# Optimization experiments

Hardware: AMD Instinct MI355X
Metric: run time of the kernel (lower is better)

The kernel has to match this reference:

```python
import jax, jax.numpy as jnp
import numpy as np

N = 100000
E = 800000
D_IN = 256
D_H = 512


def setup_inputs() -> dict:
    key = jax.random.key(0)
    ks = jax.random.split(key, 8)
    s_in = 1.0 / np.sqrt(D_IN)
    s_h = 1.0 / np.sqrt(D_H)
    return {
        "x": jax.random.normal(ks[0], (N, D_IN), jnp.float32),
        "edge_index": jax.random.randint(ks[1], (2, E), 0, N, dtype=jnp.int64),
        "W1": jax.random.normal(ks[2], (D_IN, D_H), jnp.float32) * s_in,
        "b1": jnp.zeros((D_H,), jnp.float32),
        "W2": jax.random.normal(ks[3], (D_H, D_H), jnp.float32) * s_h,
        "b2": jnp.zeros((D_H,), jnp.float32),
        "W3": jax.random.normal(ks[4], (D_H, D_H), jnp.float32) * s_h,
        "b3": jnp.zeros((D_H,), jnp.float32),
        "Wfc": jax.random.normal(ks[5], (D_H, D_IN), jnp.float32) * s_h,
        "bfc": jnp.zeros((D_IN,), jnp.float32),
    }


def _gcn_prep(edge_index, n_nodes):
    # PyG GCNConv: add self-loops, symmetric deg^{-1/2} normalization.
    loop = jnp.arange(n_nodes, dtype=edge_index.dtype)
    row = jnp.concatenate([edge_index[0], loop])  # destination
    col = jnp.concatenate([edge_index[1], loop])  # source
    deg = jax.ops.segment_sum(jnp.ones_like(row, dtype=jnp.float32), row,
                              num_segments=n_nodes)
    dinv = jax.lax.rsqrt(deg)  # deg >= 1 due to self loops
    norm = dinv[row] * dinv[col]  # [E+N]
    return row, col, norm


def _gcn_conv(x, W, b, row, col, norm, n_nodes):
    h = x @ W  # [N, out]
    msg = h[col] * norm[:, None]  # [E+N, out] gather + scale
    out = jax.ops.segment_sum(msg, row, num_segments=n_nodes)  # scatter-add
    return out + b


def reference(x, edge_index, W1, b1, W2, b2, W3, b3, Wfc, bfc):
    n = x.shape[0]
    row, col, norm = _gcn_prep(edge_index, n)
    h = jax.nn.relu(_gcn_conv(x, W1, b1, row, col, norm, n))
    h = jax.nn.relu(_gcn_conv(h, W2, b2, row, col, norm, n))
    h = jax.nn.relu(_gcn_conv(h, W3, b3, row, col, norm, n))
    return h @ Wfc + bfc
```

## Files before the change

kernel.cpp:

```cpp
#include <hip/hip_runtime.h>

#define N_NODES 100000
#define NPAD    100096
#define E_EDGES 800000
#define HALF_STRIDE ((size_t)NPAD * 256)

typedef _Float16 f16;
typedef _Float16 f16x4 __attribute__((ext_vector_type(4)));
typedef _Float16 f16x8 __attribute__((ext_vector_type(8)));
typedef float    f32x4 __attribute__((ext_vector_type(4)));

__device__ inline void async16(const void* g, void* l) {
    __builtin_amdgcn_global_load_lds(
        (const __attribute__((address_space(1))) void*)g,
        (__attribute__((address_space(3))) void*)l, 16, 0, 0);
}

__global__ void k_deg(const int* __restrict__ ei, int* __restrict__ deg) {
    int e = blockIdx.x * 256 + threadIdx.x;
    if (e < E_EDGES) atomicAdd(&deg[ei[e]], 1);
}

__global__ void k_scan1(const int* __restrict__ deg, int* __restrict__ off,
                        int* __restrict__ bsum, float* __restrict__ dinv) {
    __shared__ int s[256];
    int i = blockIdx.x * 256 + threadIdx.x;
    int v = (i < N_NODES) ? deg[i] : 0;
    if (i < N_NODES) dinv[i] = rsqrtf((float)(v + 1));
    s[threadIdx.x] = v;
    __syncthreads();
    for (int d = 1; d < 256; d <<= 1) {
        int t = (threadIdx.x >= d) ? s[threadIdx.x - d] : 0;
        __syncthreads();
        s[threadIdx.x] += t;
        __syncthreads();
    }
    if (i < N_NODES) off[i] = s[threadIdx.x] - v;
    if (threadIdx.x == 255) bsum[blockIdx.x] = s[255];
}

__global__ void k_scan2(int* __restrict__ bsum, int nb) {
    __shared__ int s[512];
    int tid = threadIdx.x;
    int v = (tid < nb) ? bsum[tid] : 0;
    s[tid] = v;
    __syncthreads();
    for (int d = 1; d < 512; d <<= 1) {
        int t = (tid >= d) ? s[tid - d] : 0;
        __syncthreads();
        s[tid] += t;
        __syncthreads();
    }
    if (tid < nb) bsum[tid] = s[tid] - v;
}

__global__ void k_scan3(int* __restrict__ off, const int* __restrict__ bsum) {
    int i = blockIdx.x * 256 + threadIdx.x;
    if (i < N_NODES) off[i] += bsum[blockIdx.x];
    if (i == 0) off[N_NODES] = E_EDGES;
}

__global__ void k_fill(const int* __restrict__ ei, const int* __restrict__ off,
                       int* __restrict__ cursor, int* __restrict__ csr) {
    int e = blockIdx.x * 256 + threadIdx.x;
    if (e >= E_EDGES) return;
    int dst = ei[e];
    int src = ei[E_EDGES + e];
    int pos = atomicAdd(&cursor[dst], 1);
    csr[off[dst] + pos] = src;
}

__global__ void k_x_to_f16(const float* __restrict__ x, f16* __restrict__ xh) {
    int i = blockIdx.x * 256 + threadIdx.x;
    if (i >= (N_NODES * 256) / 4) return;
    float4 v = ((const float4*)x)[i];
    f16x4 o;
    o.x = (f16)v.x; o.y = (f16)v.y; o.z = (f16)v.z; o.w = (f16)v.w;
    ((f16x4*)xh)[i] = o;
}

__global__ void k_transpose(const float* __restrict__ W, f16* __restrict__ Wt,
                            int K, int M) {
    int m = blockIdx.x * 256 + threadIdx.x;
    int k = blockIdx.y;
    if (m < M) Wt[(size_t)m * K + k] = (f16)W[(size_t)k * M + m];
}

template<int K, int M, int MODE, bool SPLIT>
__launch_bounds__(256, 2)
__global__ void k_gemm(const f16* __restrict__ A, const f16* __restrict__ B,
                       void* __restrict__ C, const float* __restrict__ bias) {
    __shared__ __align__(16) char smem[16384];
    f16* As = (f16*)smem;
    f16* Bs = (f16*)(smem + 8192);
    int tid  = threadIdx.x;
    int wave = tid >> 6, lane = tid & 63;
    int wr = (wave >> 1) * 64, wc = (wave & 1) * 64;
    int lm = lane & 15, q = lane >> 4;
    int rowBase = blockIdx.x * 128;
    int colBase = blockIdx.y * 128;

    f32x4 acc[4][4] = {};
    const f16* Ag = A + (size_t)rowBase * K;
    const f16* Bg = B + (size_t)colBase * K;

    int c0 = tid, c1 = tid + 256;
    for (int kt = 0; kt < K; kt += 32) {
        __syncthreads();
        async16(Ag + (size_t)(c0 >> 2) * K + kt + (c0 & 3) * 8, &As[c0 * 8]);
        async16(Ag + (size_t)(c1 >> 2) * K + kt + (c1 & 3) * 8, &As[c1 * 8]);
        async16(Bg + (size_t)(c0 >> 2) * K + kt + (c0 & 3) * 8, &Bs[c0 * 8]);
        async16(Bg + (size_t)(c1 >> 2) * K + kt + (c1 & 3) * 8, &Bs[c1 * 8]);
        __syncthreads();

        f16x8 a[4], b[4];
#pragma unroll
        for (int i = 0; i < 4; ++i) {
            a[i] = *(const f16x8*)&As[(wr + i * 16 + lm) * 32 + q * 8];
            b[i] = *(const f16x8*)&Bs[(wc + i * 16 + lm) * 32 + q * 8];
        }
#pragma unroll
        for (int i = 0; i < 4; ++i)
#pragma unroll
            for (int j = 0; j < 4; ++j)
                acc[i][j] = __builtin_amdgcn_mfma_f32_16x16x32_f16(
                    a[i], b[j], acc[i][j], 0, 0, 0);
    }

    if (MODE == 2) {
#pragma unroll
        for (int i = 0; i < 4; ++i) {
            int gr0 = rowBase + wr + i * 16 + q * 4;
#pragma unroll
            for (int j = 0; j < 4; ++j) {
                int gc = colBase + wc + j * 16 + lm;
                float bj = bias[gc];
#pragma unroll
                for (int r = 0; r < 4; ++r) {
                    int gr = gr0 + r;
                    if (gr < N_NODES)
                        ((float*)C)[(size_t)gr * M + gc] = acc[i][j][r] + bj;
                }
            }
        }
    } else {
        __syncthreads();
        f16* Ep = (f16*)smem + wave * (16 * 80);
#pragma unroll
        for (int i = 0; i < 4; ++i) {
#pragma unroll
            for (int j = 0; j < 4; ++j) {
                int colg = colBase + wc + j * 16 + lm;
#pragma unroll
                for (int r = 0; r < 4; ++r) {
                    float v = acc[i][j][r];
                    if (MODE == 1) {
                        v += bias[colg];
                        v = v > 0.f ? v : 0.f;
                    }
                    Ep[(q * 4 + r) * 80 + j * 16 + lm] = (f16)v;
                }
            }
            __syncthreads();
            int row0 = lane >> 3, c8 = lane & 7;
            f16x8 v0 = *(const f16x8*)&Ep[row0 * 80 + c8 * 8];
            f16x8 v1 = *(const f16x8*)&Ep[(row0 + 8) * 80 + c8 * 8];
            int gr0 = rowBase + wr + i * 16 + row0;
            int gc  = colBase + wc + c8 * 8;
            if (SPLIT) {
                f16* base = (f16*)C + (size_t)(gc >> 8) * HALF_STRIDE;
                int cl = gc & 255;
                *(f16x8*)&base[(size_t)gr0 * 256 + cl] = v0;
                *(f16x8*)&base[(size_t)(gr0 + 8) * 256 + cl] = v1;
            } else {
                *(f16x8*)&((f16*)C)[(size_t)gr0 * M + gc] = v0;
                *(f16x8*)&((f16*)C)[(size_t)(gr0 + 8) * M + gc] = v1;
            }
            __syncthreads();
        }
    }
}

template<int VE> struct VecT;
template<> struct VecT<4> { typedef f16x4 type; };
template<> struct VecT<8> { typedef f16x8 type; };

template<int CH, bool ACT>
__global__ void k_agg(const f16* __restrict__ t, const int* __restrict__ off,
                      const int* __restrict__ csr, const float* __restrict__ dinv,
                      const float* __restrict__ bias, f16* __restrict__ h) {
    constexpr int VE = CH / 64;
    typedef typename VecT<VE>::type vec;
    int node = blockIdx.x * 4 + (threadIdx.x >> 6);
    if (node >= N_NODES) return;
    int lane = threadIdx.x & 63;
    float di = dinv[node];

    const vec* rows = (const vec*)t;
    vec v = rows[(size_t)node * 64 + lane];
    float acc[VE];
#pragma unroll
    for (int j = 0; j < VE; ++j) acc[j] = di * (float)v[j];

    int s = off[node], e = off[node + 1];
    int idx = s;
    for (; idx + 4 <= e; idx += 4) {
        int i0 = csr[idx], i1 = csr[idx + 1], i2 = csr[idx + 2], i3 = csr[idx + 3];
        vec u0 = rows[(size_t)i0 * 64 + lane];
        vec u1 = rows[(size_t)i1 * 64 + lane];
        vec u2 = rows[(size_t)i2 * 64 + lane];
        vec u3 = rows[(size_t)i3 * 64 + lane];
        float d0 = dinv[i0], d1 = dinv[i1], d2 = dinv[i2], d3 = dinv[i3];
#pragma unroll
        for (int j = 0; j < VE; ++j)
            acc[j] += d0 * (float)u0[j] + d1 * (float)u1[j]
                    + d2 * (float)u2[j] + d3 * (float)u3[j];
    }
    for (; idx < e; ++idx) {
        int src = csr[idx];
        float dj = dinv[src];
        vec u = rows[(size_t)src * 64 + lane];
#pragma unroll
        for (int j = 0; j < VE; ++j) acc[j] += dj * (float)u[j];
    }

    vec o;
#pragma unroll
    for (int j = 0; j < VE; ++j) {
        float r = di * acc[j];
        if (ACT) {
            r += bias[lane * VE + j];
            r = r > 0.f ? r : 0.f;
        }
        o[j] = (f16)r;
    }
    ((vec*)h)[(size_t)node * 64 + lane] = o;
}

template<bool ACT>
__global__ void k_agg_split(const f16* __restrict__ t, const int* __restrict__ off,
                            const int* __restrict__ csr, const float* __restrict__ dinv,
                            const float* __restrict__ bias, f16* __restrict__ h) {
    int node = blockIdx.x * 4 + (threadIdx.x >> 6);
    if (node >= N_NODES) return;
    int half = blockIdx.y;
    int lane = threadIdx.x & 63;
    float di = dinv[node];

    const f16x4* rows = (const f16x4*)(t + (size_t)half * HALF_STRIDE);
    f16x4 v = rows[(size_t)node * 64 + lane];
    float acc[4];
#pragma unroll
    for (int j = 0; j < 4; ++j) acc[j] = di * (float)v[j];

    int s = off[node], e = off[node + 1];
    int idx = s;
    for (; idx + 4 <= e; idx += 4) {
        int i0 = csr[idx], i1 = csr[idx + 1], i2 = csr[idx + 2], i3 = csr[idx + 3];
        f16x4 u0 = rows[(size_t)i0 * 64 + lane];
        f16x4 u1 = rows[(size_t)i1 * 64 + lane];
        f16x4 u2 = rows[(size_t)i2 * 64 + lane];
        f16x4 u3 = rows[(size_t)i3 * 64 + lane];
        float d0 = dinv[i0], d1 = dinv[i1], d2 = dinv[i2], d3 = dinv[i3];
#pragma unroll
        for (int j = 0; j < 4; ++j)
            acc[j] += d0 * (float)u0[j] + d1 * (float)u1[j]
                    + d2 * (float)u2[j] + d3 * (float)u3[j];
    }
    for (; idx < e; ++idx) {
        int src = csr[idx];
        float dj = dinv[src];
        f16x4 u = rows[(size_t)src * 64 + lane];
#pragma unroll
        for (int j = 0; j < 4; ++j) acc[j] += dj * (float)u[j];
    }

    f16x4 o;
#pragma unroll
    for (int j = 0; j < 4; ++j) {
        float r = di * acc[j];
        if (ACT) {
            r += bias[half * 256 + lane * 4 + j];
            r = r > 0.f ? r : 0.f;
        }
        o[j] = (f16)r;
    }
    *(f16x4*)&h[(size_t)node * 512 + half * 256 + lane * 4] = o;
}

extern "C" void kernel_launch(void* const* d_in, const int* in_sizes, int n_in,
                              void* d_out, int out_size, void* d_ws, size_t ws_size,
                              hipStream_t stream) {
    const float* x   = (const float*)d_in[0];
    const int*   ei  = (const int*)d_in[1];
    const float* W1  = (const float*)d_in[2];
    const float* b1  = (const float*)d_in[3];
    const float* W2  = (const float*)d_in[4];
    const float* b2  = (const float*)d_in[5];
    const float* W3  = (const float*)d_in[6];
    const float* b3  = (const float*)d_in[7];
    const float* Wfc = (const float*)d_in[8];
    const float* bfc = (const float*)d_in[9];

    char* wsb = (char*)d_ws;
    size_t o = 0;
    auto alloc = [&](size_t bytes) -> void* {
        void* p = wsb + o;
        o += (bytes + 255) & ~(size_t)255;
        return p;
    };

    f16* xh   = (f16*)alloc((size_t)NPAD * 256 * 2);
    f16* t    = (f16*)alloc((size_t)NPAD * 512 * 2);
    f16* h    = (f16*)alloc((size_t)NPAD * 512 * 2);
    f16* Wt1  = (f16*)alloc(512 * 256 * 2);
    f16* Wt2  = (f16*)alloc(512 * 512 * 2);
    f16* Wt3  = (f16*)alloc(512 * 512 * 2);
    f16* Wtfc = (f16*)alloc(256 * 512 * 2);
    int* deg    = (int*)alloc(N_NODES * 4);
    float* dinv = (float*)alloc(N_NODES * 4);
    int* off    = (int*)alloc((N_NODES + 1) * 4);
    int* cursor = (int*)alloc(N_NODES * 4);
    int* bsum   = (int*)alloc(4096 * 4);
    int* csr    = (int*)alloc((size_t)E_EDGES * 4);

    f16* a1 = t;

    const int NB = (N_NODES + 255) / 256;

    hipMemsetAsync(deg, 0, N_NODES * 4, stream);
    hipMemsetAsync(cursor, 0, N_NODES * 4, stream);

    k_deg<<<(E_EDGES + 255) / 256, 256, 0, stream>>>(ei, deg);
    k_scan1<<<NB, 256, 0, stream>>>(deg, off, bsum, dinv);
    k_scan2<<<1, 512, 0, stream>>>(bsum, NB);
    k_scan3<<<NB, 256, 0, stream>>>(off, bsum);
    k_fill<<<(E_EDGES + 255) / 256, 256, 0, stream>>>(ei, off, cursor, csr);

    k_x_to_f16<<<(N_NODES * 256 / 4 + 255) / 256, 256, 0, stream>>>(x, xh);
    k_transpose<<<dim3(2, 256), 256, 0, stream>>>(W1, Wt1, 256, 512);
    k_transpose<<<dim3(2, 512), 256, 0, stream>>>(W2, Wt2, 512, 512);
    k_transpose<<<dim3(2, 512), 256, 0, stream>>>(W3, Wt3, 512, 512);
    k_transpose<<<dim3(1, 512), 256, 0, stream>>>(Wfc, Wtfc, 512, 256);

    dim3 g4(NPAD / 128, 4), g2(NPAD / 128, 2);
    const int AGG_GRID = N_NODES / 4;
    dim3 gs(AGG_GRID, 2);

    k_agg<256, false><<<AGG_GRID, 256, 0, stream>>>(xh, off, csr, dinv, nullptr, a1);
    k_gemm<256, 512, 1, false><<<g4, 256, 0, stream>>>(a1, Wt1, h, b1);
    k_gemm<512, 512, 0, true><<<g4, 256, 0, stream>>>(h, Wt2, t, nullptr);
    k_agg_split<true><<<gs, 256, 0, stream>>>(t, off, csr, dinv, b2, h);
    k_gemm<512, 512, 0, true><<<g4, 256, 0, stream>>>(h, Wt3, t, nullptr);
    k_agg_split<true><<<gs, 256, 0, stream>>>(t, off, csr, dinv, b3, h);
    k_gemm<512, 256, 2, false><<<g2, 256, 0, stream>>>(h, Wtfc, d_out, bfc);
}
```

Measured before the change: 909.9 us.

## Prescale features by source dinv, pad CSR rows to 4, drop split aggregation

```diff
diff --git a/kernel.cpp b/kernel.cpp
--- a/kernel.cpp
+++ b/kernel.cpp
@@ -3,7 +3,6 @@
 #define N_NODES 100000
 #define NPAD    100096
 #define E_EDGES 800000
-#define HALF_STRIDE ((size_t)NPAD * 256)
 
 typedef _Float16 f16;
 typedef _Float16 f16x4 __attribute__((ext_vector_type(4)));
@@ -25,17 +24,18 @@
                         int* __restrict__ bsum, float* __restrict__ dinv) {
     __shared__ int s[256];
     int i = blockIdx.x * 256 + threadIdx.x;
-    int v = (i < N_NODES) ? deg[i] : 0;
-    if (i < N_NODES) dinv[i] = rsqrtf((float)(v + 1));
-    s[threadIdx.x] = v;
+    int d = (i < N_NODES) ? deg[i] : 0;
+    int pd = (d + 3) & ~3;
+    dinv[i] = (i < N_NODES) ? rsqrtf((float)(d + 1)) : 0.f;
+    s[threadIdx.x] = pd;
     __syncthreads();
-    for (int d = 1; d < 256; d <<= 1) {
-        int t = (threadIdx.x >= d) ? s[threadIdx.x - d] : 0;
+    for (int dd = 1; dd < 256; dd <<= 1) {
+        int t = (threadIdx.x >= dd) ? s[threadIdx.x - dd] : 0;
         __syncthreads();
         s[threadIdx.x] += t;
         __syncthreads();
     }
-    if (i < N_NODES) off[i] = s[threadIdx.x] - v;
+    if (i < N_NODES) off[i] = s[threadIdx.x] - pd;
     if (threadIdx.x == 255) bsum[blockIdx.x] = s[255];
 }
 
@@ -54,10 +54,15 @@
     if (tid < nb) bsum[tid] = s[tid] - v;
 }
 
-__global__ void k_scan3(int* __restrict__ off, const int* __restrict__ bsum) {
+__global__ void k_scan3(int* __restrict__ off, const int* __restrict__ bsum,
+                        const int* __restrict__ deg, int* __restrict__ csr) {
     int i = blockIdx.x * 256 + threadIdx.x;
-    if (i < N_NODES) off[i] += bsum[blockIdx.x];
-    if (i == 0) off[N_NODES] = E_EDGES;
+    if (i >= N_NODES) return;
+    int o = off[i] + bsum[blockIdx.x];
+    off[i] = o;
+    int d = deg[i], pd = (d + 3) & ~3;
+    for (int k = d; k < pd; ++k) csr[o + k] = NPAD;
+    if (i == N_NODES - 1) off[N_NODES] = o + pd;
 }
 
 __global__ void k_fill(const int* __restrict__ ei, const int* __restrict__ off,
@@ -70,12 +75,16 @@
     csr[off[dst] + pos] = src;
 }
 
-__global__ void k_x_to_f16(const float* __restrict__ x, f16* __restrict__ xh) {
+__global__ void k_x_to_f16(const float* __restrict__ x,
+                           const float* __restrict__ dinv,
+                           f16* __restrict__ xh) {
     int i = blockIdx.x * 256 + threadIdx.x;
-    if (i >= (N_NODES * 256) / 4) return;
+    if (i >= N_NODES * 64) return;
+    float d = dinv[i >> 6];
     float4 v = ((const float4*)x)[i];
     f16x4 o;
-    o.x = (f16)v.x; o.y = (f16)v.y; o.z = (f16)v.z; o.w = (f16)v.w;
+    o.x = (f16)(v.x * d); o.y = (f16)(v.y * d);
+    o.z = (f16)(v.z * d); o.w = (f16)(v.w * d);
     ((f16x4*)xh)[i] = o;
 }
 
@@ -86,10 +95,11 @@
     if (m < M) Wt[(size_t)m * K + k] = (f16)W[(size_t)k * M + m];
 }
 
-template<int K, int M, int MODE, bool SPLIT>
+template<int K, int M, int MODE>
 __launch_bounds__(256, 2)
 __global__ void k_gemm(const f16* __restrict__ A, const f16* __restrict__ B,
-                       void* __restrict__ C, const float* __restrict__ bias) {
+                       void* __restrict__ C, const float* __restrict__ bias,
+                       const float* __restrict__ dsc) {
     __shared__ __align__(16) char smem[16384];
     f16* As = (f16*)smem;
     f16* Bs = (f16*)(smem + 8192);
@@ -148,6 +158,9 @@
         f16* Ep = (f16*)smem + wave * (16 * 80);
 #pragma unroll
         for (int i = 0; i < 4; ++i) {
+            f32x4 dr = {1.f, 1.f, 1.f, 1.f};
+            if (MODE == 3)
+                dr = *(const f32x4*)&dsc[rowBase + wr + i * 16 + q * 4];
 #pragma unroll
             for (int j = 0; j < 4; ++j) {
                 int colg = colBase + wc + j * 16 + lm;
@@ -158,6 +171,7 @@
                         v += bias[colg];
                         v = v > 0.f ? v : 0.f;
                     }
+                    if (MODE == 3) v *= dr[r];
                     Ep[(q * 4 + r) * 80 + j * 16 + lm] = (f16)v;
                 }
             }
@@ -167,15 +181,8 @@
             f16x8 v1 = *(const f16x8*)&Ep[(row0 + 8) * 80 + c8 * 8];
             int gr0 = rowBase + wr + i * 16 + row0;
             int gc  = colBase + wc + c8 * 8;
-            if (SPLIT) {
-                f16* base = (f16*)C + (size_t)(gc >> 8) * HALF_STRIDE;
-                int cl = gc & 255;
-                *(f16x8*)&base[(size_t)gr0 * 256 + cl] = v0;
-                *(f16x8*)&base[(size_t)(gr0 + 8) * 256 + cl] = v1;
-            } else {
-                *(f16x8*)&((f16*)C)[(size_t)gr0 * M + gc] = v0;
-                *(f16x8*)&((f16*)C)[(size_t)(gr0 + 8) * M + gc] = v1;
-            }
+            *(f16x8*)&((f16*)C)[(size_t)gr0 * M + gc] = v0;
+            *(f16x8*)&((f16*)C)[(size_t)(gr0 + 8) * M + gc] = v1;
             __syncthreads();
         }
     }
@@ -186,6 +193,7 @@
 template<> struct VecT<8> { typedef f16x8 type; };
 
 template<int CH, bool ACT>
+__launch_bounds__(256)
 __global__ void k_agg(const f16* __restrict__ t, const int* __restrict__ off,
                       const int* __restrict__ csr, const float* __restrict__ dinv,
                       const float* __restrict__ bias, f16* __restrict__ h) {
@@ -194,36 +202,31 @@
     int node = blockIdx.x * 4 + (threadIdx.x >> 6);
     if (node >= N_NODES) return;
     int lane = threadIdx.x & 63;
+    const vec* __restrict__ rows = (const vec*)t;
+
+    vec v = rows[node * 64 + lane];
+    float acc[VE];
+#pragma unroll
+    for (int j = 0; j < VE; ++j) acc[j] = (float)v[j];
+
+    int s = off[node], e = off[node + 1];
+    if (s < e) {
+        int4 iv = *(const int4*)&csr[s];
+        for (int idx = s; idx < e; idx += 4) {
+            int4 nxt = *(const int4*)&csr[idx + 4];
+            vec u0 = rows[iv.x * 64 + lane];
+            vec u1 = rows[iv.y * 64 + lane];
+            vec u2 = rows[iv.z * 64 + lane];
+            vec u3 = rows[iv.w * 64 + lane];
+            iv = nxt;
+#pragma unroll
+            for (int j = 0; j < VE; ++j)
+                acc[j] += ((float)u0[j] + (float)u1[j])
+                        + ((float)u2[j] + (float)u3[j]);
+        }
+    }
+
     float di = dinv[node];
-
-    const vec* rows = (const vec*)t;
-    vec v = rows[(size_t)node * 64 + lane];
-    float acc[VE];
-#pragma unroll
-    for (int j = 0; j < VE; ++j) acc[j] = di * (float)v[j];
-
-    int s = off[node], e = off[node + 1];
-    int idx = s;
-    for (; idx + 4 <= e; idx += 4) {
-        int i0 = csr[idx], i1 = csr[idx + 1], i2 = csr[idx + 2], i3 = csr[idx + 3];
-        vec u0 = rows[(size_t)i0 * 64 + lane];
-        vec u1 = rows[(size_t)i1 * 64 + lane];
-        vec u2 = rows[(size_t)i2 * 64 + lane];
-        vec u3 = rows[(size_t)i3 * 64 + lane];
-        float d0 = dinv[i0], d1 = dinv[i1], d2 = dinv[i2], d3 = dinv[i3];
-#pragma unroll
-        for (int j = 0; j < VE; ++j)
-            acc[j] += d0 * (float)u0[j] + d1 * (float)u1[j]
-                    + d2 * (float)u2[j] + d3 * (float)u3[j];
-    }
-    for (; idx < e; ++idx) {
-        int src = csr[idx];
-        float dj = dinv[src];
-        vec u = rows[(size_t)src * 64 + lane];
-#pragma unroll
-        for (int j = 0; j < VE; ++j) acc[j] += dj * (float)u[j];
-    }
-
     vec o;
 #pragma unroll
     for (int j = 0; j < VE; ++j) {
@@ -234,58 +237,7 @@
         }
         o[j] = (f16)r;
     }
-    ((vec*)h)[(size_t)node * 64 + lane] = o;
-}
-
-template<bool ACT>
-__global__ void k_agg_split(const f16* __restrict__ t, const int* __restrict__ off,
-                            const int* __restrict__ csr, const float* __restrict__ dinv,
-                            const float* __restrict__ bias, f16* __restrict__ h) {
-    int node = blockIdx.x * 4 + (threadIdx.x >> 6);
-    if (node >= N_NODES) return;
-    int half = blockIdx.y;
-    int lane = threadIdx.x & 63;
-    float di = dinv[node];
-
-    const f16x4* rows = (const f16x4*)(t + (size_t)half * HALF_STRIDE);
-    f16x4 v = rows[(size_t)node * 64 + lane];
-    float acc[4];
-#pragma unroll
-    for (int j = 0; j < 4; ++j) acc[j] = di * (float)v[j];
-
-    int s = off[node], e = off[node + 1];
-    int idx = s;
-    for (; idx + 4 <= e; idx += 4) {
-        int i0 = csr[idx], i1 = csr[idx + 1], i2 = csr[idx + 2], i3 = csr[idx + 3];
-        f16x4 u0 = rows[(size_t)i0 * 64 + lane];
-        f16x4 u1 = rows[(size_t)i1 * 64 + lane];
-        f16x4 u2 = rows[(size_t)i2 * 64 + lane];
-        f16x4 u3 = rows[(size_t)i3 * 64 + lane];
-        float d0 = dinv[i0], d1 = dinv[i1], d2 = dinv[i2], d3 = dinv[i3];
-#pragma unroll
-        for (int j = 0; j < 4; ++j)
-            acc[j] += d0 * (float)u0[j] + d1 * (float)u1[j]
-                    + d2 * (float)u2[j] + d3 * (float)u3[j];
-    }
-    for (; idx < e; ++idx) {
-        int src = csr[idx];
-        float dj = dinv[src];
-        f16x4 u = rows[(size_t)src * 64 + lane];
-#pragma unroll
-        for (int j = 0; j < 4; ++j) acc[j] += dj * (float)u[j];
-    }
-
-    f16x4 o;
-#pragma unroll
-    for (int j = 0; j < 4; ++j) {
-        float r = di * acc[j];
-        if (ACT) {
-            r += bias[half * 256 + lane * 4 + j];
-            r = r > 0.f ? r : 0.f;
-        }
-        o[j] = (f16)r;
-    }
-    *(f16x4*)&h[(size_t)node * 512 + half * 256 + lane * 4] = o;
+    ((vec*)h)[node * 64 + lane] = o;
 }
 
 extern "C" void kernel_launch(void* const* d_in, const int* in_sizes, int n_in,
@@ -310,19 +262,19 @@
         return p;
     };
 
-    f16* xh   = (f16*)alloc((size_t)NPAD * 256 * 2);
-    f16* t    = (f16*)alloc((size_t)NPAD * 512 * 2);
+    f16* xh   = (f16*)alloc((size_t)(NPAD + 1) * 256 * 2);
+    f16* t    = (f16*)alloc((size_t)(NPAD + 1) * 512 * 2);
     f16* h    = (f16*)alloc((size_t)NPAD * 512 * 2);
     f16* Wt1  = (f16*)alloc(512 * 256 * 2);
     f16* Wt2  = (f16*)alloc(512 * 512 * 2);
     f16* Wt3  = (f16*)alloc(512 * 512 * 2);
     f16* Wtfc = (f16*)alloc(256 * 512 * 2);
     int* deg    = (int*)alloc(N_NODES * 4);
-    float* dinv = (float*)alloc(N_NODES * 4);
+    float* dinv = (float*)alloc(NPAD * 4);
     int* off    = (int*)alloc((N_NODES + 1) * 4);
     int* cursor = (int*)alloc(N_NODES * 4);
     int* bsum   = (int*)alloc(4096 * 4);
-    int* csr    = (int*)alloc((size_t)E_EDGES * 4);
+    int* csr    = (int*)alloc(((size_t)E_EDGES + 3 * N_NODES + 8) * 4);
 
     f16* a1 = t;
 
@@ -330,14 +282,16 @@
 
     hipMemsetAsync(deg, 0, N_NODES * 4, stream);
     hipMemsetAsync(cursor, 0, N_NODES * 4, stream);
+    hipMemsetAsync(xh + (size_t)NPAD * 256, 0, 256 * 2, stream);
+    hipMemsetAsync(t  + (size_t)NPAD * 512, 0, 512 * 2, stream);
 
     k_deg<<<(E_EDGES + 255) / 256, 256, 0, stream>>>(ei, deg);
     k_scan1<<<NB, 256, 0, stream>>>(deg, off, bsum, dinv);
     k_scan2<<<1, 512, 0, stream>>>(bsum, NB);
-    k_scan3<<<NB, 256, 0, stream>>>(off, bsum);
+    k_scan3<<<NB, 256, 0, stream>>>(off, bsum, deg, csr);
     k_fill<<<(E_EDGES + 255) / 256, 256, 0, stream>>>(ei, off, cursor, csr);
 
-    k_x_to_f16<<<(N_NODES * 256 / 4 + 255) / 256, 256, 0, stream>>>(x, xh);
+    k_x_to_f16<<<(N_NODES * 64 + 255) / 256, 256, 0, stream>>>(x, dinv, xh);
     k_transpose<<<dim3(2, 256), 256, 0, stream>>>(W1, Wt1, 256, 512);
     k_transpose<<<dim3(2, 512), 256, 0, stream>>>(W2, Wt2, 512, 512);
     k_transpose<<<dim3(2, 512), 256, 0, stream>>>(W3, Wt3, 512, 512);
@@ -345,13 +299,12 @@
 
     dim3 g4(NPAD / 128, 4), g2(NPAD / 128, 2);
     const int AGG_GRID = N_NODES / 4;
-    dim3 gs(AGG_GRID, 2);
 
     k_agg<256, false><<<AGG_GRID, 256, 0, stream>>>(xh, off, csr, dinv, nullptr, a1);
-    k_gemm<256, 512, 1, false><<<g4, 256, 0, stream>>>(a1, Wt1, h, b1);
-    k_gemm<512, 512, 0, true><<<g4, 256, 0, stream>>>(h, Wt2, t, nullptr);
-    k_agg_split<true><<<gs, 256, 0, stream>>>(t, off, csr, dinv, b2, h);
-    k_gemm<512, 512, 0, true><<<g4, 256, 0, stream>>>(h, Wt3, t, nullptr);
-    k_agg_split<true><<<gs, 256, 0, stream>>>(t, off, csr, dinv, b3, h);
-    k_gemm<512, 256, 2, false><<<g2, 256, 0, stream>>>(h, Wtfc, d_out, bfc);
-}
+    k_gemm<256, 512, 1><<<g4, 256, 0, stream>>>(a1, Wt1, h, b1, nullptr);
+    k_gemm<512, 512, 3><<<g4, 256, 0, stream>>>(h, Wt2, t, nullptr, dinv);
+    k_agg<512, true><<<AGG_GRID, 256, 0, stream>>>(t, off, csr, dinv, b2, h);
+    k_gemm<512, 512, 3><<<g4, 256, 0, stream>>>(h, Wt3, t, nullptr, dinv);
+    k_agg<512, true><<<AGG_GRID, 256, 0, stream>>>(t, off, csr, dinv, b3, h);
+    k_gemm<512, 256, 2><<<g2, 256, 0, stream>>>(h, Wtfc, d_out, bfc, nullptr);
+}
```

Result: no change. 918.6 us (+1.0%).
